# Optimization experiments

Measured on AMD Instinct MI355X. Metric: run time of the kernel, lower is better.

## Reference

```python
import jax, jax.numpy as jnp
import numpy as np

N_ATOMS = 200000
N_BONDS = 400000
MAX_NEI = 10
N_MOLS = 8000
ATOM_FDIM = 87
BOND_FDIM = 6
HSIZE = 64
DEPTH = 3


def setup_inputs() -> dict:
    key = jax.random.key(0)
    ks = jax.random.split(key, 14)
    s = 0.05
    return {
        "atom_feat": jax.random.normal(ks[0], (N_ATOMS, ATOM_FDIM), jnp.float32),
        "bond_feat": jax.random.normal(ks[1], (N_BONDS, BOND_FDIM), jnp.float32),
        "atom_graph": jax.random.randint(ks[2], (N_ATOMS, MAX_NEI), 0, N_ATOMS),
        "bond_graph": jax.random.randint(ks[3], (N_ATOMS, MAX_NEI), 0, N_BONDS),
        "mol_ids": jnp.sort(jax.random.randint(ks[4], (N_ATOMS,), 0, N_MOLS)),
        # Linear weights stored as [in, out]; torch Linear has no bias here (bias=False).
        "W_atom_emb": s * jax.random.normal(ks[5], (ATOM_FDIM, HSIZE), jnp.float32),
        "W_bond_emb": s * jax.random.normal(ks[6], (BOND_FDIM, HSIZE), jnp.float32),
        "U1": s * jax.random.normal(ks[7], (HSIZE, HSIZE), jnp.float32),
        "U2": s * jax.random.normal(ks[8], (HSIZE, HSIZE), jnp.float32),
        "V": s * jax.random.normal(ks[9], (2 * HSIZE, HSIZE), jnp.float32),
        "W0": s * jax.random.normal(ks[10], (HSIZE, HSIZE), jnp.float32),
        "W1": s * jax.random.normal(ks[11], (HSIZE, HSIZE), jnp.float32),
        "W2": s * jax.random.normal(ks[12], (HSIZE, HSIZE), jnp.float32),
    }


def reference(atom_feat, bond_feat, W_atom_emb, W_bond_emb, U1, U2, V, W0, W1, W2,
              atom_graph, bond_graph, mol_ids):
    h_atom = atom_feat @ W_atom_emb            # [N, H]
    h_bond = bond_feat @ W_bond_emb            # [E, H]
    c_atom = None
    for _ in range(DEPTH):
        h_atom_nei = h_atom[atom_graph]        # [N, K, H] gather (index_select_ND)
        h_bond_nei = h_bond[bond_graph]        # [N, K, H]
        f_atom = h_atom @ W0                   # [N, H]
        f_bond_nei = h_bond_nei @ W1           # [N, K, H]
        f_atom_nei = h_atom_nei @ W2           # [N, K, H]
        c_atom = f_atom * jnp.sum(f_atom_nei * f_bond_nei, axis=1)
        nei_label = jax.nn.relu(
            jnp.concatenate([h_bond_nei, h_atom_nei], axis=-1) @ V
        ).sum(axis=1)                          # [N, H]
        h_atom = jax.nn.relu(h_atom @ U1 + nei_label @ U2)
        # dropout is identity at inference
    # scope pooling: ragged per-molecule sum over contiguous atom slices
    c_mol = jax.ops.segment_sum(c_atom, mol_ids, num_segments=N_MOLS)  # [M, H]
    return (c_mol, c_atom)
```

## Files before the change

### kernel.cpp

```cpp
#include <hip/hip_runtime.h>
#include <hip/hip_fp16.h>

#define N_ATOMS 200000
#define N_BONDS 400000
#define MAX_NEI 10
#define N_MOLS  8000
#define AFD 87
#define BFD 6
#define H 64
#define WPB 16
#define RPW 4
#define RPB (WPB*RPW)
#define NG  (RPW*MAX_NEI)

#define NT_LD(p)     __builtin_nontemporal_load(p)
#define NT_ST(p, v)  __builtin_nontemporal_store((v), (p))

__global__ __launch_bounds__(256) void k_tiny(
    const float* __restrict__ Wb, const float* __restrict__ V1,
    const float* __restrict__ W1, float* __restrict__ M1, float* __restrict__ M2)
{
    int t = threadIdx.x;
    for (int idx = t; idx < BFD * H; idx += 256) {
        int k = idx >> 6, h = idx & 63;
        float a1 = 0.f, a2 = 0.f;
        for (int j = 0; j < H; ++j) {
            float w = Wb[k * H + j];
            a1 = fmaf(w, V1[j * H + h], a1);
            a2 = fmaf(w, W1[j * H + h], a2);
        }
        M1[idx] = a1;
        M2[idx] = a2;
    }
}

__global__ __launch_bounds__(1024, 8) void k_atom_emb(
    const float* __restrict__ af, const float* __restrict__ Wemb,
    const float* __restrict__ V2, float* __restrict__ h_atom,
    __half* __restrict__ g_atom)
{
    __shared__ float sW[AFD * H];
    __shared__ float sV[H * H];
    __shared__ float sT[WPB * AFD * 4];
    int tid = threadIdx.x;
    for (int t = tid; t < AFD * H / 4; t += 1024)
        ((float4*)sW)[t] = ((const float4*)Wemb)[t];
    ((float4*)sV)[tid] = ((const float4*)V2)[tid];
    int w = tid >> 6, h = tid & 63;
    int row0 = __builtin_amdgcn_readfirstlane((int)(blockIdx.x * RPB + w * RPW));
    float* myT = sT + w * (AFD * 4);
    for (int c = h; c < AFD; c += 64) {
#pragma unroll
        for (int i = 0; i < RPW; ++i)
            myT[c * 4 + i] = NT_LD(&af[(size_t)(row0 + i) * AFD + c]);
    }
    __syncthreads();
    const float4* myTv = (const float4*)myT;
    float a0 = 0.f, a1 = 0.f, a2 = 0.f, a3 = 0.f;
#pragma unroll 4
    for (int k = 0; k < AFD; ++k) {
        float u = sW[k * H + h];
        float4 s = myTv[k];
        a0 = fmaf(s.x, u, a0); a1 = fmaf(s.y, u, a1);
        a2 = fmaf(s.z, u, a2); a3 = fmaf(s.w, u, a3);
    }
    NT_ST(&h_atom[(size_t)(row0 + 0) * H + h], a0);
    NT_ST(&h_atom[(size_t)(row0 + 1) * H + h], a1);
    NT_ST(&h_atom[(size_t)(row0 + 2) * H + h], a2);
    NT_ST(&h_atom[(size_t)(row0 + 3) * H + h], a3);
    ((float4*)myT)[h] = make_float4(a0, a1, a2, a3);
    float g0 = 0.f, g1 = 0.f, g2 = 0.f, g3 = 0.f;
#pragma unroll 4
    for (int k = 0; k < H; ++k) {
        float v = sV[k * H + h];
        float4 s = myTv[k];
        g0 = fmaf(s.x, v, g0); g1 = fmaf(s.y, v, g1);
        g2 = fmaf(s.z, v, g2); g3 = fmaf(s.w, v, g3);
    }
    g_atom[(size_t)(row0 + 0) * H + h] = __float2half(g0);
    g_atom[(size_t)(row0 + 1) * H + h] = __float2half(g1);
    g_atom[(size_t)(row0 + 2) * H + h] = __float2half(g2);
    g_atom[(size_t)(row0 + 3) * H + h] = __float2half(g3);
}

#define GATHER_NEI(i, OUT) do {                                              \
    float a = 0.f;                                                           \
    _Pragma("unroll")                                                        \
    for (int k = 0; k < MAX_NEI; ++k) {                                      \
        int ia = __builtin_amdgcn_readlane(my_ia, (i) * MAX_NEI + k);        \
        int ib = __builtin_amdgcn_readlane(my_ib, (i) * MAX_NEI + k);        \
        float ga = __half2float(g_atom[(size_t)ia * H + h]);                 \
        const float* bp = bf + (size_t)ib * BFD;                             \
        float gb = 0.f;                                                      \
        _Pragma("unroll")                                                    \
        for (int j = 0; j < BFD; ++j) gb = fmaf(bp[j], m1c[j], gb);          \
        a += fmaxf(gb + ga, 0.f);                                            \
    }                                                                        \
    OUT = a;                                                                 \
} while (0)

__global__ __launch_bounds__(1024, 8) void k_update(
    const float* __restrict__ h_in, const __half* __restrict__ g_atom,
    const float* __restrict__ bf, const float* __restrict__ M1,
    const int* __restrict__ ag, const int* __restrict__ bg,
    const float* __restrict__ U1, const float* __restrict__ U2,
    const float* __restrict__ Mx,
    float* __restrict__ h_out, __half* __restrict__ extra_out)
{
    __shared__ float sU1[H * H];
    __shared__ float sU2[H * H];
    __shared__ float4 sRow[WPB][H];
    __shared__ float4 sNei[WPB][H];
    int tid = threadIdx.x;
    ((float4*)sU1)[tid] = ((const float4*)U1)[tid];
    ((float4*)sU2)[tid] = ((const float4*)U2)[tid];
    int w = tid >> 6, h = tid & 63;
    int row0 = __builtin_amdgcn_readfirstlane((int)(blockIdx.x * RPB + w * RPW));

    int my_ia = 0, my_ib = 0;
    if (h < NG) {
        my_ia = ag[(size_t)row0 * MAX_NEI + h];
        my_ib = bg[(size_t)row0 * MAX_NEI + h];
    }
    float m1c[BFD];
#pragma unroll
    for (int j = 0; j < BFD; ++j) m1c[j] = M1[j * H + h];
    float x0 = NT_LD(&h_in[(size_t)(row0 + 0) * H + h]);
    float x1 = NT_LD(&h_in[(size_t)(row0 + 1) * H + h]);
    float x2 = NT_LD(&h_in[(size_t)(row0 + 2) * H + h]);
    float x3 = NT_LD(&h_in[(size_t)(row0 + 3) * H + h]);
    sRow[w][h] = make_float4(x0, x1, x2, x3);
    float n0, n1, n2, n3;
    GATHER_NEI(0, n0);
    GATHER_NEI(1, n1);
    GATHER_NEI(2, n2);
    GATHER_NEI(3, n3);
    sNei[w][h] = make_float4(n0, n1, n2, n3);
    __syncthreads();
    float o0 = 0.f, o1 = 0.f, o2 = 0.f, o3 = 0.f;
#pragma unroll 4
    for (int k = 0; k < H; ++k) {
        float u = sU1[k * H + h];
        float4 s = sRow[w][k];
        o0 = fmaf(s.x, u, o0); o1 = fmaf(s.y, u, o1);
        o2 = fmaf(s.z, u, o2); o3 = fmaf(s.w, u, o3);
    }
#pragma unroll 4
    for (int k = 0; k < H; ++k) {
        float u = sU2[k * H + h];
        float4 s = sNei[w][k];
        o0 = fmaf(s.x, u, o0); o1 = fmaf(s.y, u, o1);
        o2 = fmaf(s.z, u, o2); o3 = fmaf(s.w, u, o3);
    }
    o0 = fmaxf(o0, 0.f); o1 = fmaxf(o1, 0.f);
    o2 = fmaxf(o2, 0.f); o3 = fmaxf(o3, 0.f);
    NT_ST(&h_out[(size_t)(row0 + 0) * H + h], o0);
    NT_ST(&h_out[(size_t)(row0 + 1) * H + h], o1);
    NT_ST(&h_out[(size_t)(row0 + 2) * H + h], o2);
    NT_ST(&h_out[(size_t)(row0 + 3) * H + h], o3);
    sRow[w][h] = make_float4(o0, o1, o2, o3);
    float g0 = 0.f, g1 = 0.f, g2 = 0.f, g3 = 0.f;
#pragma unroll 4
    for (int k = 0; k < H; ++k) {
        float u = Mx[k * H + h];
        float4 s = sRow[w][k];
        g0 = fmaf(s.x, u, g0); g1 = fmaf(s.y, u, g1);
        g2 = fmaf(s.z, u, g2); g3 = fmaf(s.w, u, g3);
    }
    extra_out[(size_t)(row0 + 0) * H + h] = __float2half(g0);
    extra_out[(size_t)(row0 + 1) * H + h] = __float2half(g1);
    extra_out[(size_t)(row0 + 2) * H + h] = __float2half(g2);
    extra_out[(size_t)(row0 + 3) * H + h] = __float2half(g3);
}

#define GATHER_PROD(i, OUT) do {                                             \
    float a = 0.f;                                                           \
    _Pragma("unroll")                                                        \
    for (int k = 0; k < MAX_NEI; ++k) {                                      \
        int ia = __builtin_amdgcn_readlane(my_ia, (i) * MAX_NEI + k);        \
        int ib = __builtin_amdgcn_readlane(my_ib, (i) * MAX_NEI + k);        \
        float pa = __half2float(p_atom[(size_t)ia * H + h]);                 \
        const float* bp = bf + (size_t)ib * BFD;                             \
        float pb = 0.f;                                                      \
        _Pragma("unroll")                                                    \
        for (int j = 0; j < BFD; ++j) pb = fmaf(bp[j], m2c[j], pb);          \
        a = fmaf(pa, pb, a);                                                 \
    }                                                                        \
    OUT = a;                                                                 \
} while (0)

__global__ __launch_bounds__(1024, 8) void k_catom(
    const float* __restrict__ h2, const __half* __restrict__ p_atom,
    const float* __restrict__ bf, const float* __restrict__ M2,
    const int* __restrict__ ag, const int* __restrict__ bg,
    const float* __restrict__ W0, float* __restrict__ c_atom)
{
    __shared__ float sW[H * H];
    __shared__ float4 sRow[WPB][H];
    int tid = threadIdx.x;
    ((float4*)sW)[tid] = ((const float4*)W0)[tid];
    int w = tid >> 6, h = tid & 63;
    int row0 = __builtin_amdgcn_readfirstlane((int)(blockIdx.x * RPB + w * RPW));

    int my_ia = 0, my_ib = 0;
    if (h < NG) {
        my_ia = ag[(size_t)row0 * MAX_NEI + h];
        my_ib = bg[(size_t)row0 * MAX_NEI + h];
    }
    float m2c[BFD];
#pragma unroll
    for (int j = 0; j < BFD; ++j) m2c[j] = M2[j * H + h];
    float x0 = NT_LD(&h2[(size_t)(row0 + 0) * H + h]);
    float x1 = NT_LD(&h2[(size_t)(row0 + 1) * H + h]);
    float x2 = NT_LD(&h2[(size_t)(row0 + 2) * H + h]);
    float x3 = NT_LD(&h2[(size_t)(row0 + 3) * H + h]);
    sRow[w][h] = make_float4(x0, x1, x2, x3);
    float s0, s1, s2, s3;
    GATHER_PROD(0, s0);
    GATHER_PROD(1, s1);
    GATHER_PROD(2, s2);
    GATHER_PROD(3, s3);
    __syncthreads();
    float f0 = 0.f, f1 = 0.f, f2 = 0.f, f3 = 0.f;
#pragma unroll 4
    for (int k = 0; k < H; ++k) {
        float u = sW[k * H + h];
        float4 s = sRow[w][k];
        f0 = fmaf(s.x, u, f0); f1 = fmaf(s.y, u, f1);
        f2 = fmaf(s.z, u, f2); f3 = fmaf(s.w, u, f3);
    }
    c_atom[(size_t)(row0 + 0) * H + h] = f0 * s0;
    c_atom[(size_t)(row0 + 1) * H + h] = f1 * s1;
    c_atom[(size_t)(row0 + 2) * H + h] = f2 * s2;
    c_atom[(size_t)(row0 + 3) * H + h] = f3 * s3;
}

__global__ void k_segsum(
    const float* __restrict__ c_atom, const int* __restrict__ mol_ids,
    float* __restrict__ c_mol)
{
    int m = blockIdx.x;
    int h = threadIdx.x;
    int lo = 0, hi = N_ATOMS;
    while (lo < hi) { int mid = (lo + hi) >> 1; if (mol_ids[mid] < m) lo = mid + 1; else hi = mid; }
    int start = lo;
    hi = N_ATOMS;
    while (lo < hi) { int mid = (lo + hi) >> 1; if (mol_ids[mid] < m + 1) lo = mid + 1; else hi = mid; }
    int end = lo;
    float acc = 0.f;
    for (int a = start; a < end; ++a) acc += c_atom[a * H + h];
    c_mol[m * H + h] = acc;
}

extern "C" void kernel_launch(void* const* d_in, const int* in_sizes, int n_in,
                              void* d_out, int out_size, void* d_ws, size_t ws_size,
                              hipStream_t stream)
{
    const float* atom_feat = (const float*)d_in[0];
    const float* bond_feat = (const float*)d_in[1];
    const int*   ag        = (const int*)d_in[2];
    const int*   bg        = (const int*)d_in[3];
    const int*   mol_ids   = (const int*)d_in[4];
    const float* W_aemb    = (const float*)d_in[5];
    const float* W_bemb    = (const float*)d_in[6];
    const float* U1        = (const float*)d_in[7];
    const float* U2        = (const float*)d_in[8];
    const float* V         = (const float*)d_in[9];
    const float* W0        = (const float*)d_in[10];
    const float* W1        = (const float*)d_in[11];
    const float* W2        = (const float*)d_in[12];

    float* out    = (float*)d_out;
    float* c_mol  = out;
    float* c_atom = out + (size_t)N_MOLS * H;

    float*  hA  = (float*)d_ws;
    __half* gA0 = (__half*)(hA + (size_t)N_ATOMS * H);
    float*  M1  = (float*)(gA0 + (size_t)N_ATOMS * H);
    float*  M2  = M1 + BFD * H;
    __half* gA1 = (__half*)c_atom;

    const float* V1 = V;
    const float* V2 = V + H * H;

    k_tiny<<<1, 256, 0, stream>>>(W_bemb, V1, W1, M1, M2);

    k_atom_emb<<<N_ATOMS / RPB, 1024, 0, stream>>>(atom_feat, W_aemb, V2, hA, gA0);

    k_update<<<N_ATOMS / RPB, 1024, 0, stream>>>(hA, gA0, bond_feat, M1, ag, bg,
                                                 U1, U2, V2, hA, gA1);
    k_update<<<N_ATOMS / RPB, 1024, 0, stream>>>(hA, gA1, bond_feat, M1, ag, bg,
                                                 U1, U2, W2, hA, gA0);

    k_catom<<<N_ATOMS / RPB, 1024, 0, stream>>>(hA, gA0, bond_feat, M2, ag, bg,
                                                W0, c_atom);

    k_segsum<<<N_MOLS, 64, 0, stream>>>(c_atom, mol_ids, c_mol);
}
```

Measured before the change: 726.2 us.

## Store hidden state in fp16 and gather neighbor pairs with dword loads plus shuffles

```diff
diff --git a/kernel.cpp b/kernel.cpp
--- a/kernel.cpp
+++ b/kernel.cpp
@@ -36,7 +36,7 @@
 
 __global__ __launch_bounds__(1024, 8) void k_atom_emb(
     const float* __restrict__ af, const float* __restrict__ Wemb,
-    const float* __restrict__ V2, float* __restrict__ h_atom,
+    const float* __restrict__ V2, unsigned short* __restrict__ h_atom,
     __half* __restrict__ g_atom)
 {
     __shared__ float sW[AFD * H];
@@ -64,10 +64,10 @@
         a0 = fmaf(s.x, u, a0); a1 = fmaf(s.y, u, a1);
         a2 = fmaf(s.z, u, a2); a3 = fmaf(s.w, u, a3);
     }
-    NT_ST(&h_atom[(size_t)(row0 + 0) * H + h], a0);
-    NT_ST(&h_atom[(size_t)(row0 + 1) * H + h], a1);
-    NT_ST(&h_atom[(size_t)(row0 + 2) * H + h], a2);
-    NT_ST(&h_atom[(size_t)(row0 + 3) * H + h], a3);
+    NT_ST(&h_atom[(size_t)(row0 + 0) * H + h], __builtin_bit_cast(unsigned short, __float2half(a0)));
+    NT_ST(&h_atom[(size_t)(row0 + 1) * H + h], __builtin_bit_cast(unsigned short, __float2half(a1)));
+    NT_ST(&h_atom[(size_t)(row0 + 2) * H + h], __builtin_bit_cast(unsigned short, __float2half(a2)));
+    NT_ST(&h_atom[(size_t)(row0 + 3) * H + h], __builtin_bit_cast(unsigned short, __float2half(a3)));
     ((float4*)myT)[h] = make_float4(a0, a1, a2, a3);
     float g0 = 0.f, g1 = 0.f, g2 = 0.f, g3 = 0.f;
 #pragma unroll 4
@@ -83,29 +83,52 @@
     g_atom[(size_t)(row0 + 3) * H + h] = __float2half(g3);
 }
 
-#define GATHER_NEI(i, OUT) do {                                              \
-    float a = 0.f;                                                           \
+#define PLOAD(SRC, g_, p_, DW) do {                                          \
+    int _iaA = __builtin_amdgcn_readlane(my_ia, (g_) * MAX_NEI + 2 * (p_));  \
+    int _iaB = __builtin_amdgcn_readlane(my_ia, (g_) * MAX_NEI + 2 * (p_) + 1);\
+    unsigned _off = (unsigned)(h < 32 ? _iaA : _iaB) * (unsigned)(H * 2)     \
+                    + (unsigned)(h & 31) * 4u;                               \
+    DW = *(const unsigned*)((const char*)(SRC) + _off);                      \
+} while (0)
+
+#define BDOT(MC, g_, p_, G1, G2) do {                                        \
+    int _ibA = __builtin_amdgcn_readlane(my_ib, (g_) * MAX_NEI + 2 * (p_));  \
+    int _ibB = __builtin_amdgcn_readlane(my_ib, (g_) * MAX_NEI + 2 * (p_) + 1);\
+    const float* _b1 = bf + (size_t)_ibA * BFD;                              \
+    const float* _b2 = bf + (size_t)_ibB * BFD;                              \
+    G1 = 0.f; G2 = 0.f;                                                      \
     _Pragma("unroll")                                                        \
-    for (int k = 0; k < MAX_NEI; ++k) {                                      \
-        int ia = __builtin_amdgcn_readlane(my_ia, (i) * MAX_NEI + k);        \
-        int ib = __builtin_amdgcn_readlane(my_ib, (i) * MAX_NEI + k);        \
-        float ga = __half2float(g_atom[(size_t)ia * H + h]);                 \
-        const float* bp = bf + (size_t)ib * BFD;                             \
-        float gb = 0.f;                                                      \
-        _Pragma("unroll")                                                    \
-        for (int j = 0; j < BFD; ++j) gb = fmaf(bp[j], m1c[j], gb);          \
-        a += fmaxf(gb + ga, 0.f);                                            \
+    for (int _j = 0; _j < BFD; ++_j) {                                       \
+        G1 = fmaf(_b1[_j], MC[_j], G1);                                      \
+        G2 = fmaf(_b2[_j], MC[_j], G2);                                      \
     }                                                                        \
-    OUT = a;                                                                 \
 } while (0)
 
+#define CONS_NEI(DW, G1, G2, ACC) do {                                       \
+    unsigned _d1 = (unsigned)__shfl((int)(DW), (h >> 1), 64);                \
+    unsigned _d2 = (unsigned)__shfl((int)(DW), 32 + (h >> 1), 64);           \
+    unsigned short _u1 = (unsigned short)(_d1 >> ((h & 1) * 16));            \
+    unsigned short _u2 = (unsigned short)(_d2 >> ((h & 1) * 16));            \
+    ACC += fmaxf(G1 + __half2float(__builtin_bit_cast(__half, _u1)), 0.f);   \
+    ACC += fmaxf(G2 + __half2float(__builtin_bit_cast(__half, _u2)), 0.f);   \
+} while (0)
+
+#define CONS_PROD(DW, G1, G2, ACC) do {                                      \
+    unsigned _d1 = (unsigned)__shfl((int)(DW), (h >> 1), 64);                \
+    unsigned _d2 = (unsigned)__shfl((int)(DW), 32 + (h >> 1), 64);           \
+    unsigned short _u1 = (unsigned short)(_d1 >> ((h & 1) * 16));            \
+    unsigned short _u2 = (unsigned short)(_d2 >> ((h & 1) * 16));            \
+    ACC = fmaf(__half2float(__builtin_bit_cast(__half, _u1)), G1, ACC);      \
+    ACC = fmaf(__half2float(__builtin_bit_cast(__half, _u2)), G2, ACC);      \
+} while (0)
+
 __global__ __launch_bounds__(1024, 8) void k_update(
-    const float* __restrict__ h_in, const __half* __restrict__ g_atom,
+    const unsigned short* __restrict__ h_in, const __half* __restrict__ g_atom,
     const float* __restrict__ bf, const float* __restrict__ M1,
     const int* __restrict__ ag, const int* __restrict__ bg,
     const float* __restrict__ U1, const float* __restrict__ U2,
     const float* __restrict__ Mx,
-    float* __restrict__ h_out, __half* __restrict__ extra_out)
+    unsigned short* __restrict__ h_out, __half* __restrict__ extra_out)
 {
     __shared__ float sU1[H * H];
     __shared__ float sU2[H * H];
@@ -125,16 +148,41 @@
     float m1c[BFD];
 #pragma unroll
     for (int j = 0; j < BFD; ++j) m1c[j] = M1[j * H + h];
-    float x0 = NT_LD(&h_in[(size_t)(row0 + 0) * H + h]);
-    float x1 = NT_LD(&h_in[(size_t)(row0 + 1) * H + h]);
-    float x2 = NT_LD(&h_in[(size_t)(row0 + 2) * H + h]);
-    float x3 = NT_LD(&h_in[(size_t)(row0 + 3) * H + h]);
+    float x0 = __half2float(__builtin_bit_cast(__half, NT_LD(&h_in[(size_t)(row0 + 0) * H + h])));
+    float x1 = __half2float(__builtin_bit_cast(__half, NT_LD(&h_in[(size_t)(row0 + 1) * H + h])));
+    float x2 = __half2float(__builtin_bit_cast(__half, NT_LD(&h_in[(size_t)(row0 + 2) * H + h])));
+    float x3 = __half2float(__builtin_bit_cast(__half, NT_LD(&h_in[(size_t)(row0 + 3) * H + h])));
     sRow[w][h] = make_float4(x0, x1, x2, x3);
-    float n0, n1, n2, n3;
-    GATHER_NEI(0, n0);
-    GATHER_NEI(1, n1);
-    GATHER_NEI(2, n2);
-    GATHER_NEI(3, n3);
+
+    unsigned dwa0, dwa1, dwa2, dwa3;
+    float ga0_1, ga0_2, ga1_1, ga1_2, ga2_1, ga2_2, ga3_1, ga3_2;
+    PLOAD(g_atom, 0, 0, dwa0); PLOAD(g_atom, 1, 0, dwa1);
+    PLOAD(g_atom, 2, 0, dwa2); PLOAD(g_atom, 3, 0, dwa3);
+    BDOT(m1c, 0, 0, ga0_1, ga0_2); BDOT(m1c, 1, 0, ga1_1, ga1_2);
+    BDOT(m1c, 2, 0, ga2_1, ga2_2); BDOT(m1c, 3, 0, ga3_1, ga3_2);
+    float n0 = 0.f, n1 = 0.f, n2 = 0.f, n3 = 0.f;
+#pragma unroll
+    for (int p = 0; p < MAX_NEI / 2; ++p) {
+        unsigned dwb0, dwb1, dwb2, dwb3;
+        float gb0_1, gb0_2, gb1_1, gb1_2, gb2_1, gb2_2, gb3_1, gb3_2;
+        if (p < MAX_NEI / 2 - 1) {
+            PLOAD(g_atom, 0, p + 1, dwb0); PLOAD(g_atom, 1, p + 1, dwb1);
+            PLOAD(g_atom, 2, p + 1, dwb2); PLOAD(g_atom, 3, p + 1, dwb3);
+            BDOT(m1c, 0, p + 1, gb0_1, gb0_2); BDOT(m1c, 1, p + 1, gb1_1, gb1_2);
+            BDOT(m1c, 2, p + 1, gb2_1, gb2_2); BDOT(m1c, 3, p + 1, gb3_1, gb3_2);
+        } else {
+            dwb0 = dwb1 = dwb2 = dwb3 = 0u;
+            gb0_1 = gb0_2 = gb1_1 = gb1_2 = 0.f;
+            gb2_1 = gb2_2 = gb3_1 = gb3_2 = 0.f;
+        }
+        CONS_NEI(dwa0, ga0_1, ga0_2, n0);
+        CONS_NEI(dwa1, ga1_1, ga1_2, n1);
+        CONS_NEI(dwa2, ga2_1, ga2_2, n2);
+        CONS_NEI(dwa3, ga3_1, ga3_2, n3);
+        dwa0 = dwb0; dwa1 = dwb1; dwa2 = dwb2; dwa3 = dwb3;
+        ga0_1 = gb0_1; ga0_2 = gb0_2; ga1_1 = gb1_1; ga1_2 = gb1_2;
+        ga2_1 = gb2_1; ga2_2 = gb2_2; ga3_1 = gb3_1; ga3_2 = gb3_2;
+    }
     sNei[w][h] = make_float4(n0, n1, n2, n3);
     __syncthreads();
     float o0 = 0.f, o1 = 0.f, o2 = 0.f, o3 = 0.f;
@@ -154,10 +202,10 @@
     }
     o0 = fmaxf(o0, 0.f); o1 = fmaxf(o1, 0.f);
     o2 = fmaxf(o2, 0.f); o3 = fmaxf(o3, 0.f);
-    NT_ST(&h_out[(size_t)(row0 + 0) * H + h], o0);
-    NT_ST(&h_out[(size_t)(row0 + 1) * H + h], o1);
-    NT_ST(&h_out[(size_t)(row0 + 2) * H + h], o2);
-    NT_ST(&h_out[(size_t)(row0 + 3) * H + h], o3);
+    NT_ST(&h_out[(size_t)(row0 + 0) * H + h], __builtin_bit_cast(unsigned short, __float2half(o0)));
+    NT_ST(&h_out[(size_t)(row0 + 1) * H + h], __builtin_bit_cast(unsigned short, __float2half(o1)));
+    NT_ST(&h_out[(size_t)(row0 + 2) * H + h], __builtin_bit_cast(unsigned short, __float2half(o2)));
+    NT_ST(&h_out[(size_t)(row0 + 3) * H + h], __builtin_bit_cast(unsigned short, __float2half(o3)));
     sRow[w][h] = make_float4(o0, o1, o2, o3);
     float g0 = 0.f, g1 = 0.f, g2 = 0.f, g3 = 0.f;
 #pragma unroll 4
@@ -173,24 +221,8 @@
     extra_out[(size_t)(row0 + 3) * H + h] = __float2half(g3);
 }
 
-#define GATHER_PROD(i, OUT) do {                                             \
-    float a = 0.f;                                                           \
-    _Pragma("unroll")                                                        \
-    for (int k = 0; k < MAX_NEI; ++k) {                                      \
-        int ia = __builtin_amdgcn_readlane(my_ia, (i) * MAX_NEI + k);        \
-        int ib = __builtin_amdgcn_readlane(my_ib, (i) * MAX_NEI + k);        \
-        float pa = __half2float(p_atom[(size_t)ia * H + h]);                 \
-        const float* bp = bf + (size_t)ib * BFD;                             \
-        float pb = 0.f;                                                      \
-        _Pragma("unroll")                                                    \
-        for (int j = 0; j < BFD; ++j) pb = fmaf(bp[j], m2c[j], pb);          \
-        a = fmaf(pa, pb, a);                                                 \
-    }                                                                        \
-    OUT = a;                                                                 \
-} while (0)
-
 __global__ __launch_bounds__(1024, 8) void k_catom(
-    const float* __restrict__ h2, const __half* __restrict__ p_atom,
+    const unsigned short* __restrict__ h2, const __half* __restrict__ p_atom,
     const float* __restrict__ bf, const float* __restrict__ M2,
     const int* __restrict__ ag, const int* __restrict__ bg,
     const float* __restrict__ W0, float* __restrict__ c_atom)
@@ -210,16 +242,41 @@
     float m2c[BFD];
 #pragma unroll
     for (int j = 0; j < BFD; ++j) m2c[j] = M2[j * H + h];
-    float x0 = NT_LD(&h2[(size_t)(row0 + 0) * H + h]);
-    float x1 = NT_LD(&h2[(size_t)(row0 + 1) * H + h]);
-    float x2 = NT_LD(&h2[(size_t)(row0 + 2) * H + h]);
-    float x3 = NT_LD(&h2[(size_t)(row0 + 3) * H + h]);
+    float x0 = __half2float(__builtin_bit_cast(__half, NT_LD(&h2[(size_t)(row0 + 0) * H + h])));
+    float x1 = __half2float(__builtin_bit_cast(__half, NT_LD(&h2[(size_t)(row0 + 1) * H + h])));
+    float x2 = __half2float(__builtin_bit_cast(__half, NT_LD(&h2[(size_t)(row0 + 2) * H + h])));
+    float x3 = __half2float(__builtin_bit_cast(__half, NT_LD(&h2[(size_t)(row0 + 3) * H + h])));
     sRow[w][h] = make_float4(x0, x1, x2, x3);
-    float s0, s1, s2, s3;
-    GATHER_PROD(0, s0);
-    GATHER_PROD(1, s1);
-    GATHER_PROD(2, s2);
-    GATHER_PROD(3, s3);
+
+    unsigned dwa0, dwa1, dwa2, dwa3;
+    float ga0_1, ga0_2, ga1_1, ga1_2, ga2_1, ga2_2, ga3_1, ga3_2;
+    PLOAD(p_atom, 0, 0, dwa0); PLOAD(p_atom, 1, 0, dwa1);
+    PLOAD(p_atom, 2, 0, dwa2); PLOAD(p_atom, 3, 0, dwa3);
+    BDOT(m2c, 0, 0, ga0_1, ga0_2); BDOT(m2c, 1, 0, ga1_1, ga1_2);
+    BDOT(m2c, 2, 0, ga2_1, ga2_2); BDOT(m2c, 3, 0, ga3_1, ga3_2);
+    float s0 = 0.f, s1 = 0.f, s2 = 0.f, s3 = 0.f;
+#pragma unroll
+    for (int p = 0; p < MAX_NEI / 2; ++p) {
+        unsigned dwb0, dwb1, dwb2, dwb3;
+        float gb0_1, gb0_2, gb1_1, gb1_2, gb2_1, gb2_2, gb3_1, gb3_2;
+        if (p < MAX_NEI / 2 - 1) {
+            PLOAD(p_atom, 0, p + 1, dwb0); PLOAD(p_atom, 1, p + 1, dwb1);
+            PLOAD(p_atom, 2, p + 1, dwb2); PLOAD(p_atom, 3, p + 1, dwb3);
+            BDOT(m2c, 0, p + 1, gb0_1, gb0_2); BDOT(m2c, 1, p + 1, gb1_1, gb1_2);
+            BDOT(m2c, 2, p + 1, gb2_1, gb2_2); BDOT(m2c, 3, p + 1, gb3_1, gb3_2);
+        } else {
+            dwb0 = dwb1 = dwb2 = dwb3 = 0u;
+            gb0_1 = gb0_2 = gb1_1 = gb1_2 = 0.f;
+            gb2_1 = gb2_2 = gb3_1 = gb3_2 = 0.f;
+        }
+        CONS_PROD(dwa0, ga0_1, ga0_2, s0);
+        CONS_PROD(dwa1, ga1_1, ga1_2, s1);
+        CONS_PROD(dwa2, ga2_1, ga2_2, s2);
+        CONS_PROD(dwa3, ga3_1, ga3_2, s3);
+        dwa0 = dwb0; dwa1 = dwb1; dwa2 = dwb2; dwa3 = dwb3;
+        ga0_1 = gb0_1; ga0_2 = gb0_2; ga1_1 = gb1_1; ga1_2 = gb1_2;
+        ga2_1 = gb2_1; ga2_2 = gb2_2; ga3_1 = gb3_1; ga3_2 = gb3_2;
+    }
     __syncthreads();
     float f0 = 0.f, f1 = 0.f, f2 = 0.f, f3 = 0.f;
 #pragma unroll 4
@@ -274,7 +331,7 @@
     float* c_mol  = out;
     float* c_atom = out + (size_t)N_MOLS * H;
 
-    float*  hA  = (float*)d_ws;
+    unsigned short* hA = (unsigned short*)d_ws;
     __half* gA0 = (__half*)(hA + (size_t)N_ATOMS * H);
     float*  M1  = (float*)(gA0 + (size_t)N_ATOMS * H);
     float*  M2  = M1 + BFD * H;
```

New measurement: 691.6 us (median of 2 runs). 1.05x faster.
